# Performance work log

Hardware: AMD Instinct MI355X
Metric: run time of the kernel (lower is better)

## Reference

```python
import jax, jax.numpy as jnp
import numpy as np

HIDDEN_DIM = 128

def setup_inputs() -> dict:
    key = jax.random.key(0)
    kq, kk, kv = jax.random.split(key, 3)
    B, S, D = 32, 2048, HIDDEN_DIM
    q = jax.random.normal(kq, (B, S, D), dtype=jnp.float32)
    k = jax.random.normal(kk, (B, S, D), dtype=jnp.float32)
    v = jax.random.normal(kv, (B, S, D), dtype=jnp.float32)
    return {"q": q, "k": k, "v": v}

def reference(q, k, v):
    # scores: [B, Sq, Sk]
    scale = jnp.asarray(np.sqrt(1.0 / HIDDEN_DIM), dtype=q.dtype)
    scores = jnp.einsum('bqd,bkd->bqk', q, k) * scale
    attention = jax.nn.softmax(scores, axis=2)  # dropout p=0.0 -> identity
    context = jnp.einsum('bqk,bkd->bqd', attention, v)
    return (context, attention)
```

## Files before the change

kernel.cpp:

```cpp
#include <hip/hip_runtime.h>

typedef _Float16 half8 __attribute__((ext_vector_type(8)));
typedef float f32x16 __attribute__((ext_vector_type(16)));
typedef float f32x4v __attribute__((ext_vector_type(4)));

constexpr int S  = 2048;
constexpr int D  = 128;
constexpr int TQ = 32;
constexpr int NW = 8;
constexpr int CPW = S / NW;
constexpr int NT  = CPW / 32;
constexpr float SCALE = 0.08838834764831845f;

__launch_bounds__(512, 2)
__global__ void attn_fwd(const float* __restrict__ Q,
                         const float* __restrict__ K,
                         const float* __restrict__ V,
                         float* __restrict__ Oc,
                         float* __restrict__ Oa) {
    const int b    = blockIdx.y;
    const int q0   = blockIdx.x * TQ;
    const int tid  = threadIdx.x;
    const int wave = tid >> 6;
    const int lane = tid & 63;
    const int l31  = lane & 31;
    const int hl   = lane >> 5;

    __shared__ _Float16 Pch[TQ][CPW + 8];
    __shared__ float red[NW][TQ];
    __shared__ float gmax[TQ];
    __shared__ float grs[TQ];
    __shared__ float cpart[4][TQ][32];

    const float* qrow = Q + ((size_t)b * S + (q0 + l31)) * D;
    half8 qf[8];
#pragma unroll
    for (int s = 0; s < 8; ++s) {
        const int d0 = s * 16 + hl * 8;
        f32x4v a = *(const f32x4v*)(qrow + d0);
        f32x4v c = *(const f32x4v*)(qrow + d0 + 4);
        qf[s][0] = (_Float16)a[0]; qf[s][1] = (_Float16)a[1];
        qf[s][2] = (_Float16)a[2]; qf[s][3] = (_Float16)a[3];
        qf[s][4] = (_Float16)c[0]; qf[s][5] = (_Float16)c[1];
        qf[s][6] = (_Float16)c[2]; qf[s][7] = (_Float16)c[3];
    }

    const float* kbase = K + (size_t)b * S * D;
    f32x16 acc[NT];
#pragma unroll
    for (int t = 0; t < NT; ++t) {
        f32x16 a;
#pragma unroll
        for (int r = 0; r < 16; ++r) a[r] = 0.0f;
        const float* krow = kbase + (size_t)(wave * CPW + t * 32 + l31) * D;
#pragma unroll
        for (int s = 0; s < 8; ++s) {
            const int d0 = s * 16 + hl * 8;
            f32x4v x = *(const f32x4v*)(krow + d0);
            f32x4v y = *(const f32x4v*)(krow + d0 + 4);
            half8 kf;
            kf[0] = (_Float16)x[0]; kf[1] = (_Float16)x[1];
            kf[2] = (_Float16)x[2]; kf[3] = (_Float16)x[3];
            kf[4] = (_Float16)y[0]; kf[5] = (_Float16)y[1];
            kf[6] = (_Float16)y[2]; kf[7] = (_Float16)y[3];
            a = __builtin_amdgcn_mfma_f32_32x32x16_f16(qf[s], kf, a, 0, 0, 0);
        }
        acc[t] = a;
    }

    float mx[16];
#pragma unroll
    for (int r = 0; r < 16; ++r) {
        float m = -1e30f;
#pragma unroll
        for (int t = 0; t < NT; ++t) {
            acc[t][r] *= SCALE;
            m = fmaxf(m, acc[t][r]);
        }
#pragma unroll
        for (int off = 1; off < 32; off <<= 1)
            m = fmaxf(m, __shfl_xor(m, off, 64));
        mx[r] = m;
    }
    if (l31 < 16)
        red[wave][(l31 & 3) + 8 * (l31 >> 2) + 4 * hl] = mx[l31];
    __syncthreads();
    if (tid < TQ) {
        float m = red[0][tid];
#pragma unroll
        for (int w = 1; w < NW; ++w) m = fmaxf(m, red[w][tid]);
        gmax[tid] = m;
    }
    __syncthreads();

    float sm[16];
#pragma unroll
    for (int r = 0; r < 16; ++r) {
        const int row = (r & 3) + 8 * (r >> 2) + 4 * hl;
        const float g = gmax[row];
        float s = 0.0f;
#pragma unroll
        for (int t = 0; t < NT; ++t) {
            float p = __expf(acc[t][r] - g);
            acc[t][r] = p;
            s += p;
        }
#pragma unroll
        for (int off = 1; off < 32; off <<= 1)
            s += __shfl_xor(s, off, 64);
        sm[r] = s;
    }
    if (l31 < 16)
        red[wave][(l31 & 3) + 8 * (l31 >> 2) + 4 * hl] = sm[l31];
    __syncthreads();
    if (tid < TQ) {
        float s = 0.0f;
#pragma unroll
        for (int w = 0; w < NW; ++w) s += red[w][tid];
        grs[tid] = 1.0f / s;
    }
    __syncthreads();

    float* arow_base = Oa + ((size_t)b * S + q0) * S + wave * CPW;
#pragma unroll
    for (int r = 0; r < 16; ++r) {
        const int row = (r & 3) + 8 * (r >> 2) + 4 * hl;
        const float rv = grs[row];
        float* ar = arow_base + (size_t)row * S;
#pragma unroll
        for (int t = 0; t < NT; ++t) {
            float pn = acc[t][r] * rv;
            acc[t][r] = pn;
            ar[t * 32 + l31] = pn;
        }
    }

    const float* vbase = V + (size_t)b * S * D;
    const int dtile = wave & 3;
    const int khalf = wave >> 2;
    const int dcol  = dtile * 32 + l31;
    f32x16 ctx;
#pragma unroll
    for (int r = 0; r < 16; ++r) ctx[r] = 0.0f;

    for (int cw = 0; cw < NW; ++cw) {
        __syncthreads();
        if (wave == cw) {
#pragma unroll
            for (int r = 0; r < 16; ++r) {
                const int row = (r & 3) + 8 * (r >> 2) + 4 * hl;
#pragma unroll
                for (int t = 0; t < NT; ++t)
                    Pch[row][t * 32 + l31] = (_Float16)acc[t][r];
            }
        }
        __syncthreads();
#pragma unroll
        for (int s = 0; s < 8; ++s) {
            const int kk = khalf * 128 + s * 16 + hl * 8;
            half8 pf = *(const half8*)(&Pch[l31][kk]);
            half8 vf;
#pragma unroll
            for (int j = 0; j < 8; ++j)
                vf[j] = (_Float16)vbase[(size_t)(cw * CPW + kk + j) * D + dcol];
            ctx = __builtin_amdgcn_mfma_f32_32x32x16_f16(pf, vf, ctx, 0, 0, 0);
        }
    }

    __syncthreads();
    if (khalf == 1) {
#pragma unroll
        for (int r = 0; r < 16; ++r) {
            const int row = (r & 3) + 8 * (r >> 2) + 4 * hl;
            cpart[dtile][row][l31] = ctx[r];
        }
    }
    __syncthreads();
    if (khalf == 0) {
#pragma unroll
        for (int r = 0; r < 16; ++r) {
            const int row = (r & 3) + 8 * (r >> 2) + 4 * hl;
            float vsum = ctx[r] + cpart[dtile][row][l31];
            Oc[((size_t)b * S + q0 + row) * D + dcol] = vsum;
        }
    }
}

extern "C" void kernel_launch(void* const* d_in, const int* in_sizes, int n_in,
                              void* d_out, int out_size, void* d_ws, size_t ws_size,
                              hipStream_t stream) {
    const float* q = (const float*)d_in[0];
    const float* k = (const float*)d_in[1];
    const float* v = (const float*)d_in[2];
    const int B = in_sizes[0] / (S * D);
    float* ctx  = (float*)d_out;
    float* attn = ctx + (size_t)B * S * D;
    dim3 grid(S / TQ, B);
    attn_fwd<<<grid, dim3(512), 0, stream>>>(q, k, v, ctx, attn);
}
```

Measured before the change: 1.102 ms.

## Switch to 16x16 MFMA with 16 waves, double-buffered P slices and XCD swizzle

Restructures the kernel to 1024-thread blocks of 16 waves. Each wave owns a 16-query by 256-key tile and uses the 16x16x32 MFMA instead of 32x32x16, which cuts per-wave accumulator registers. The PV stage no longer splits K across waves, so the LDS cross-wave reduction of context partials goes away. P slices are now double-buffered, halving the barriers per chunk. A block-index swizzle over 8 groups groups neighbouring query blocks of one batch on the same XCD to improve K/V L2 reuse. The risks are the larger block size, uncoalesced strided V loads, and whether 4 blocks per CU is reachable.

```diff
diff --git a/kernel.cpp b/kernel.cpp
--- a/kernel.cpp
+++ b/kernel.cpp
@@ -1,76 +1,79 @@
 #include <hip/hip_runtime.h>
 
 typedef _Float16 half8 __attribute__((ext_vector_type(8)));
-typedef float f32x16 __attribute__((ext_vector_type(16)));
-typedef float f32x4v __attribute__((ext_vector_type(4)));
+typedef _Float16 half4 __attribute__((ext_vector_type(4)));
+typedef float    f32x4v __attribute__((ext_vector_type(4)));
 
-constexpr int S  = 2048;
-constexpr int D  = 128;
-constexpr int TQ = 32;
-constexpr int NW = 8;
-constexpr int CPW = S / NW;
-constexpr int NT  = CPW / 32;
+constexpr int S    = 2048;
+constexpr int D    = 128;
+constexpr int TQ   = 32;
+constexpr int QB   = S / TQ;
+constexpr int CPW  = 256;
+constexpr int NT   = CPW / 16;
+constexpr int PPAD = 8;
 constexpr float SCALE = 0.08838834764831845f;
 
-__launch_bounds__(512, 2)
+__launch_bounds__(1024, 4)
 __global__ void attn_fwd(const float* __restrict__ Q,
                          const float* __restrict__ K,
                          const float* __restrict__ V,
                          float* __restrict__ Oc,
-                         float* __restrict__ Oa) {
-    const int b    = blockIdx.y;
-    const int q0   = blockIdx.x * TQ;
+                         float* __restrict__ Oa)
+{
+    const int nper = gridDim.x >> 3;
+    const int bid  = blockIdx.x;
+    const int swz  = (bid & 7) * nper + (bid >> 3);
+    const int b    = swz / QB;
+    const int q0   = (swz % QB) * TQ;
+
     const int tid  = threadIdx.x;
     const int wave = tid >> 6;
+    const int wr   = wave >> 3;
+    const int wc   = wave & 7;
     const int lane = tid & 63;
-    const int l31  = lane & 31;
-    const int hl   = lane >> 5;
+    const int l15  = lane & 15;
+    const int g    = lane >> 4;
 
-    __shared__ _Float16 Pch[TQ][CPW + 8];
-    __shared__ float red[NW][TQ];
+    __shared__ _Float16 Pbuf[2][TQ][CPW + PPAD];
+    __shared__ float red[16][16];
     __shared__ float gmax[TQ];
     __shared__ float grs[TQ];
-    __shared__ float cpart[4][TQ][32];
 
-    const float* qrow = Q + ((size_t)b * S + (q0 + l31)) * D;
-    half8 qf[8];
+    const float* qrow = Q + ((size_t)b * S + (q0 + wr * 16 + l15)) * D;
+    half8 qf[4];
 #pragma unroll
-    for (int s = 0; s < 8; ++s) {
-        const int d0 = s * 16 + hl * 8;
+    for (int ks = 0; ks < 4; ++ks) {
+        const int d0 = ks * 32 + g * 8;
         f32x4v a = *(const f32x4v*)(qrow + d0);
         f32x4v c = *(const f32x4v*)(qrow + d0 + 4);
-        qf[s][0] = (_Float16)a[0]; qf[s][1] = (_Float16)a[1];
-        qf[s][2] = (_Float16)a[2]; qf[s][3] = (_Float16)a[3];
-        qf[s][4] = (_Float16)c[0]; qf[s][5] = (_Float16)c[1];
-        qf[s][6] = (_Float16)c[2]; qf[s][7] = (_Float16)c[3];
+        half8 h;
+        h[0]=(_Float16)a[0]; h[1]=(_Float16)a[1]; h[2]=(_Float16)a[2]; h[3]=(_Float16)a[3];
+        h[4]=(_Float16)c[0]; h[5]=(_Float16)c[1]; h[6]=(_Float16)c[2]; h[7]=(_Float16)c[3];
+        qf[ks] = h;
     }
 
     const float* kbase = K + (size_t)b * S * D;
-    f32x16 acc[NT];
+    f32x4v acc[NT];
+#pragma unroll
+    for (int t = 0; t < NT; ++t) { acc[t][0]=0.f; acc[t][1]=0.f; acc[t][2]=0.f; acc[t][3]=0.f; }
 #pragma unroll
     for (int t = 0; t < NT; ++t) {
-        f32x16 a;
+        const float* krow = kbase + (size_t)(wc * CPW + t * 16 + l15) * D;
 #pragma unroll
-        for (int r = 0; r < 16; ++r) a[r] = 0.0f;
-        const float* krow = kbase + (size_t)(wave * CPW + t * 32 + l31) * D;
-#pragma unroll
-        for (int s = 0; s < 8; ++s) {
-            const int d0 = s * 16 + hl * 8;
+        for (int ks = 0; ks < 4; ++ks) {
+            const int d0 = ks * 32 + g * 8;
             f32x4v x = *(const f32x4v*)(krow + d0);
             f32x4v y = *(const f32x4v*)(krow + d0 + 4);
             half8 kf;
-            kf[0] = (_Float16)x[0]; kf[1] = (_Float16)x[1];
-            kf[2] = (_Float16)x[2]; kf[3] = (_Float16)x[3];
-            kf[4] = (_Float16)y[0]; kf[5] = (_Float16)y[1];
-            kf[6] = (_Float16)y[2]; kf[7] = (_Float16)y[3];
-            a = __builtin_amdgcn_mfma_f32_32x32x16_f16(qf[s], kf, a, 0, 0, 0);
+            kf[0]=(_Float16)x[0]; kf[1]=(_Float16)x[1]; kf[2]=(_Float16)x[2]; kf[3]=(_Float16)x[3];
+            kf[4]=(_Float16)y[0]; kf[5]=(_Float16)y[1]; kf[6]=(_Float16)y[2]; kf[7]=(_Float16)y[3];
+            acc[t] = __builtin_amdgcn_mfma_f32_16x16x32_f16(qf[ks], kf, acc[t], 0, 0, 0);
         }
-        acc[t] = a;
     }
 
-    float mx[16];
+    float mx[4];
 #pragma unroll
-    for (int r = 0; r < 16; ++r) {
+    for (int r = 0; r < 4; ++r) {
         float m = -1e30f;
 #pragma unroll
         for (int t = 0; t < NT; ++t) {
@@ -78,112 +81,107 @@
             m = fmaxf(m, acc[t][r]);
         }
 #pragma unroll
-        for (int off = 1; off < 32; off <<= 1)
+        for (int off = 1; off < 16; off <<= 1)
             m = fmaxf(m, __shfl_xor(m, off, 64));
         mx[r] = m;
     }
-    if (l31 < 16)
-        red[wave][(l31 & 3) + 8 * (l31 >> 2) + 4 * hl] = mx[l31];
+    if (l15 == 0) {
+#pragma unroll
+        for (int r = 0; r < 4; ++r) red[wave][g * 4 + r] = mx[r];
+    }
     __syncthreads();
     if (tid < TQ) {
-        float m = red[0][tid];
+        const int wr_ = tid >> 4, lr = tid & 15;
+        float m = red[wr_ * 8][lr];
 #pragma unroll
-        for (int w = 1; w < NW; ++w) m = fmaxf(m, red[w][tid]);
+        for (int w = 1; w < 8; ++w) m = fmaxf(m, red[wr_ * 8 + w][lr]);
         gmax[tid] = m;
     }
     __syncthreads();
 
-    float sm[16];
+    float sm[4];
 #pragma unroll
-    for (int r = 0; r < 16; ++r) {
-        const int row = (r & 3) + 8 * (r >> 2) + 4 * hl;
-        const float g = gmax[row];
+    for (int r = 0; r < 4; ++r) {
+        const float gm = gmax[wr * 16 + g * 4 + r];
         float s = 0.0f;
 #pragma unroll
         for (int t = 0; t < NT; ++t) {
-            float p = __expf(acc[t][r] - g);
+            float p = __expf(acc[t][r] - gm);
             acc[t][r] = p;
             s += p;
         }
 #pragma unroll
-        for (int off = 1; off < 32; off <<= 1)
+        for (int off = 1; off < 16; off <<= 1)
             s += __shfl_xor(s, off, 64);
         sm[r] = s;
     }
-    if (l31 < 16)
-        red[wave][(l31 & 3) + 8 * (l31 >> 2) + 4 * hl] = sm[l31];
+    if (l15 == 0) {
+#pragma unroll
+        for (int r = 0; r < 4; ++r) red[wave][g * 4 + r] = sm[r];
+    }
     __syncthreads();
     if (tid < TQ) {
+        const int wr_ = tid >> 4, lr = tid & 15;
         float s = 0.0f;
 #pragma unroll
-        for (int w = 0; w < NW; ++w) s += red[w][tid];
+        for (int w = 0; w < 8; ++w) s += red[wr_ * 8 + w][lr];
         grs[tid] = 1.0f / s;
     }
     __syncthreads();
 
-    float* arow_base = Oa + ((size_t)b * S + q0) * S + wave * CPW;
+    float rv[4];
 #pragma unroll
-    for (int r = 0; r < 16; ++r) {
-        const int row = (r & 3) + 8 * (r >> 2) + 4 * hl;
-        const float rv = grs[row];
-        float* ar = arow_base + (size_t)row * S;
+    for (int r = 0; r < 4; ++r) rv[r] = grs[wr * 16 + g * 4 + r];
+
+    float* oab = Oa + ((size_t)b * S + q0 + wr * 16) * S + wc * CPW;
+    half4 ph[NT];
 #pragma unroll
-        for (int t = 0; t < NT; ++t) {
-            float pn = acc[t][r] * rv;
-            acc[t][r] = pn;
-            ar[t * 32 + l31] = pn;
+    for (int t = 0; t < NT; ++t) {
+        const int c = t * 16 + l15;
+#pragma unroll
+        for (int r = 0; r < 4; ++r) {
+            float pn = acc[t][r] * rv[r];
+            ph[t][r] = (_Float16)pn;
+            oab[(size_t)(g * 4 + r) * S + c] = pn;
         }
     }
 
-    const float* vbase = V + (size_t)b * S * D;
-    const int dtile = wave & 3;
-    const int khalf = wave >> 2;
-    const int dcol  = dtile * 32 + l31;
-    f32x16 ctx;
+    auto write_slice = [&](int bi) {
 #pragma unroll
-    for (int r = 0; r < 16; ++r) ctx[r] = 0.0f;
+        for (int t = 0; t < NT; ++t) {
+            const int c = t * 16 + l15;
+#pragma unroll
+            for (int r = 0; r < 4; ++r)
+                Pbuf[bi][wr * 16 + g * 4 + r][c] = ph[t][r];
+        }
+    };
 
-    for (int cw = 0; cw < NW; ++cw) {
-        __syncthreads();
-        if (wave == cw) {
+    const float* vb0 = V + (size_t)b * S * D + (wc * 16 + l15);
+    f32x4v ctx; ctx[0]=0.f; ctx[1]=0.f; ctx[2]=0.f; ctx[3]=0.f;
+
+    if (wc == 0) write_slice(0);
+    __syncthreads();
+
+    for (int cw = 0; cw < 8; ++cw) {
+        if (wc == cw + 1) write_slice((cw + 1) & 1);
+        const _Float16* prow = &Pbuf[cw & 1][wr * 16 + l15][g * 8];
+        const float* vb = vb0 + (size_t)(cw * CPW + g * 8) * D;
 #pragma unroll
-            for (int r = 0; r < 16; ++r) {
-                const int row = (r & 3) + 8 * (r >> 2) + 4 * hl;
-#pragma unroll
-                for (int t = 0; t < NT; ++t)
-                    Pch[row][t * 32 + l31] = (_Float16)acc[t][r];
-            }
-        }
-        __syncthreads();
-#pragma unroll
-        for (int s = 0; s < 8; ++s) {
-            const int kk = khalf * 128 + s * 16 + hl * 8;
-            half8 pf = *(const half8*)(&Pch[l31][kk]);
+        for (int mf = 0; mf < 8; ++mf) {
+            half8 pf = *(const half8*)(prow + mf * 32);
             half8 vf;
 #pragma unroll
             for (int j = 0; j < 8; ++j)
-                vf[j] = (_Float16)vbase[(size_t)(cw * CPW + kk + j) * D + dcol];
-            ctx = __builtin_amdgcn_mfma_f32_32x32x16_f16(pf, vf, ctx, 0, 0, 0);
+                vf[j] = (_Float16)vb[(size_t)(mf * 32 + j) * D];
+            ctx = __builtin_amdgcn_mfma_f32_16x16x32_f16(pf, vf, ctx, 0, 0, 0);
         }
+        __syncthreads();
     }
 
-    __syncthreads();
-    if (khalf == 1) {
+    float* ocb = Oc + ((size_t)b * S + q0 + wr * 16) * D + (wc * 16 + l15);
 #pragma unroll
-        for (int r = 0; r < 16; ++r) {
-            const int row = (r & 3) + 8 * (r >> 2) + 4 * hl;
-            cpart[dtile][row][l31] = ctx[r];
-        }
-    }
-    __syncthreads();
-    if (khalf == 0) {
-#pragma unroll
-        for (int r = 0; r < 16; ++r) {
-            const int row = (r & 3) + 8 * (r >> 2) + 4 * hl;
-            float vsum = ctx[r] + cpart[dtile][row][l31];
-            Oc[((size_t)b * S + q0 + row) * D + dcol] = vsum;
-        }
-    }
+    for (int r = 0; r < 4; ++r)
+        ocb[(size_t)(g * 4 + r) * D] = ctx[r];
 }
 
 extern "C" void kernel_launch(void* const* d_in, const int* in_sizes, int n_in,
@@ -195,6 +193,6 @@
     const int B = in_sizes[0] / (S * D);
     float* ctx  = (float*)d_out;
     float* attn = ctx + (size_t)B * S * D;
-    dim3 grid(S / TQ, B);
-    attn_fwd<<<grid, dim3(512), 0, stream>>>(q, k, v, ctx, attn);
+    dim3 grid(B * QB);
+    attn_fwd<<<grid, dim3(1024), 0, stream>>>(q, k, v, ctx, attn);
 }
```

Measured after the change: 1.325 ms. +20.2%, slower.
